# Kernel tuning notes

Hardware: AMD Instinct MI355X
Metric: run time of the kernel (lower is better)

The kernel has to match this reference:

```python
import jax, jax.numpy as jnp
import numpy as np

B, S, D = 4, 4096, 2048
K, H = 64, 32
HD = K // H  # 2
LN_EPS = 1e-5


def setup_inputs() -> dict:
    key = jax.random.key(0)
    ks = jax.random.split(key, 8)
    def xavier(k, shape):
        fan_in, fan_out = shape[1], shape[0]
        lim = float(np.sqrt(6.0 / (fan_in + fan_out)))
        return jax.random.uniform(k, shape, jnp.float32, -lim, lim)
    return {
        "x": jax.random.normal(ks[0], (B, S, D), jnp.float32),
        "norm_w": jnp.ones((D,), jnp.float32),
        "norm_b": jnp.zeros((D,), jnp.float32),
        "qkv_w": xavier(ks[1], (3 * K, D)),
        "qkv_b": jnp.zeros((3 * K,), jnp.float32),
        "fm_w": xavier(ks[2], (HD, HD)),
        "fm_b": jnp.zeros((HD,), jnp.float32),
        "out_w": xavier(ks[3], (D, K)),
        "out_b": jnp.zeros((D,), jnp.float32),
    }


def reference(x, norm_w, norm_b, qkv_w, qkv_b, fm_w, fm_b, out_w, out_b):
    # LayerNorm
    mu = jnp.mean(x, axis=-1, keepdims=True)
    var = jnp.var(x, axis=-1, keepdims=True)
    xn = (x - mu) * jax.lax.rsqrt(var + LN_EPS) * norm_w + norm_b
    # QKV projection: [B,S,3K]
    qkv = xn @ qkv_w.T + qkv_b
    q, k, v = jnp.split(qkv, 3, axis=-1)
    # [B,S,K] -> [B,H,S,hd]
    def heads(t):
        return t.reshape(B, S, H, HD).transpose(0, 2, 1, 3)
    q, k, v = heads(q), heads(k), heads(v)
    # feature map: ReLU(Linear)
    q = jax.nn.relu(q @ fm_w.T + fm_b)
    k = jax.nn.relu(k @ fm_w.T + fm_b)
    # linear attention: kv state [B,H,hd,hd]
    kv = jnp.einsum('bhsd,bhse->bhde', k, v)
    attn = jnp.einsum('bhsd,bhde->bhse', q, kv)
    k_sum = jnp.sum(k, axis=2)                      # [B,H,hd]
    q_k_sum = jnp.einsum('bhsd,bhd->bhs', q, k_sum)[..., None]
    attn = attn / (q_k_sum + 1e-8)
    # merge heads -> [B,S,K]
    attn = attn.transpose(0, 2, 1, 3).reshape(B, S, K)
    out = attn @ out_w.T + out_b
    return x + out
```

## Files before the change

kernel.cpp:

```cpp
#include <hip/hip_runtime.h>
#include <hip/hip_bf16.h>
#include <stdint.h>

typedef unsigned short ushort_t;

#define BB 4
#define SS 4096
#define DD 2048
#define KKC 64
#define HH 32
#define NT (BB*SS)
#define NQKV 192
#define QB 64

#define BUFSZ 40960
#define XOFF  24576

typedef float f32x4 __attribute__((ext_vector_type(4)));
typedef short s16x8 __attribute__((ext_vector_type(8)));

__device__ __forceinline__ ushort_t f2bf(float f) {
    union { float f; uint32_t u; } c; c.f = f;
    uint32_t u = c.u + 0x7fffu + ((c.u >> 16) & 1u);
    return (ushort_t)(u >> 16);
}
__device__ __forceinline__ float bf2f(ushort_t b) {
    union { uint32_t u; float f; } c; c.u = (uint32_t)b << 16; return c.f;
}

__device__ __forceinline__ uint32_t cvtpk(float lo, float hi) {
    uint32_t r;
    asm("v_cvt_pk_bf16_f32 %0, %1, %2" : "=v"(r) : "v"(lo), "v"(hi));
    return r;
}

__device__ __forceinline__ void mfma16(f32x4& d, s16x8 a, s16x8 b) {
    asm volatile("v_mfma_f32_16x16x32_bf16 %0, %1, %2, %0" : "+v"(d) : "v"(a), "v"(b));
}

__device__ __forceinline__ void gload_lds16(const void* gsrc, void* ldst) {
    __builtin_amdgcn_global_load_lds(
        (const __attribute__((address_space(1))) unsigned int*)gsrc,
        (__attribute__((address_space(3))) unsigned int*)ldst,
        16, 0, 0);
}

__global__ __launch_bounds__(256) void k_pre(
    const float* __restrict__ qkv_w, const float* __restrict__ nw,
    const float* __restrict__ out_w,
    ushort_t* __restrict__ W1, ushort_t* __restrict__ W2) {
    int E = blockIdx.x * 256 + threadIdx.x;
    if (E < 49152) {
        int lane = E & 63; int rest = E >> 6;
        int f = rest % 12, g = rest / 12;
        int col = f * 16 + (lane & 15);
        int k0 = g * 32 + 8 * (lane >> 4);
        const float* src = qkv_w + (size_t)col * DD + k0;
        const float* wp = nw + k0;
        union { ushort_t u[8]; uint4 v; } cv;
        #pragma unroll
        for (int e = 0; e < 8; ++e) cv.u[e] = f2bf(src[e] * wp[e]);
        *(uint4*)(W1 + (size_t)E * 8) = cv.v;
    } else {
        int E2 = E - 49152;
        int lane = E2 & 63; int rest = E2 >> 6;
        int kk = rest & 1, F = rest >> 1;
        int n = F * 16 + (lane & 15);
        int k0 = kk * 32 + 8 * (lane >> 4);
        const float* src = out_w + (size_t)n * KKC + k0;
        union { ushort_t u[8]; uint4 v; } cv;
        #pragma unroll
        for (int e = 0; e < 8; ++e) cv.u[e] = f2bf(src[e]);
        *(uint4*)(W2 + (size_t)E2 * 8) = cv.v;
    }
}

__global__ __launch_bounds__(256) void k_colsum(
    const float* __restrict__ qkv_w, const float* __restrict__ nw,
    const float* __restrict__ nb, const float* __restrict__ qkv_b,
    float* __restrict__ S, float* __restrict__ qb2) {
    int col = blockIdx.x * 4 + (threadIdx.x >> 6);
    int lane = threadIdx.x & 63;
    float s = 0.f, qb = 0.f;
    for (int j = 0; j < 32; ++j) {
        int k = j * 64 + lane;
        float w = qkv_w[(size_t)col * DD + k];
        s += bf2f(f2bf(w * nw[k]));
        qb += nb[k] * w;
    }
    #pragma unroll
    for (int off = 32; off >= 1; off >>= 1) {
        s += __shfl_xor(s, off);
        qb += __shfl_xor(qb, off);
    }
    if (lane == 0) { S[col] = s; qb2[col] = qb + qkv_b[col]; }
}

__global__ __launch_bounds__(512) void k_qkv(
    const float* __restrict__ x, const ushort_t* __restrict__ W1,
    const float* __restrict__ S, const float* __restrict__ qb2,
    const float* __restrict__ fm_w, const float* __restrict__ fm_b,
    float* __restrict__ qfeat,
    float* __restrict__ kvpart)
{
    extern __shared__ __align__(16) char dynlds[];
    __shared__ float kvred[32][16][6];
    __shared__ float stats2[2][QB][2];
    __shared__ float stats[QB][2];

    const int tid = threadIdx.x;
    const int wave = tid >> 6, lane = tid & 63;
    const int rg = wave & 3, ch = wave >> 2;
    const int m0 = blockIdx.x * QB;

    const int rloc = rg * 16 + (lane & 15);
    const int q4 = lane >> 4;
    const int swz = rloc & 7;
    const int fbase = ch * 6;

    const int idx0 = wave * 64 + lane;
    const int idx1 = 512 + idx0;
    const int row0 = idx0 >> 4, row1 = idx1 >> 4;
    const size_t xg0 = (size_t)(m0 + row0) * DD + (((idx0 & 15) ^ (row0 & 7)) * 4);
    const size_t xg1 = (size_t)(m0 + row1) * DD + (((idx1 & 15) ^ (row1 & 7)) * 4);
    const int xd0 = idx0 * 16 - lane * 16;
    const int xd1 = idx1 * 16 - lane * 16;

    f32x4 acc[6];
    #pragma unroll
    for (int j = 0; j < 6; ++j) acc[j] = (f32x4){0.f, 0.f, 0.f, 0.f};
    float st1 = 0.f, st2 = 0.f;

#define STAGE(T, OB) do { \
        char* bB_ = dynlds + (OB); \
        char* bX_ = dynlds + (OB) + XOFF; \
        _Pragma("unroll") \
        for (int i_ = 0; i_ < 3; ++i_) { \
            int eb_ = i_ * 512 + wave * 64; \
            gload_lds16((const char*)W1 + ((size_t)(T) * 1536 + eb_ + lane) * 16, \
                        bB_ + eb_ * 16); \
        } \
        gload_lds16(x + xg0 + (size_t)(T) * 64, bX_ + xd0); \
        gload_lds16(x + xg1 + (size_t)(T) * 64, bX_ + xd1); \
    } while (0)

#define STEP_BODY(OC, T) do { \
        const s16x8* bb_ = (const s16x8*)(dynlds + (OC)); \
        const float* xb_ = (const float*)(dynlds + (OC) + XOFF) + rloc * 64; \
        const bool doStats_ = (((T) & 1) == ch); \
        s16x8 afr0_, afr1_; \
        { \
            int sg0_ = 2 * q4, sg1_ = 8 + 2 * q4; \
            float4 a0_ = *(const float4*)(xb_ + ((sg0_    ) ^ swz) * 4); \
            float4 a1_ = *(const float4*)(xb_ + ((sg0_ + 1) ^ swz) * 4); \
            float4 b0_ = *(const float4*)(xb_ + ((sg1_    ) ^ swz) * 4); \
            float4 b1_ = *(const float4*)(xb_ + ((sg1_ + 1) ^ swz) * 4); \
            if (doStats_) { \
                st1 += a0_.x+a0_.y+a0_.z+a0_.w + a1_.x+a1_.y+a1_.z+a1_.w \
                     + b0_.x+b0_.y+b0_.z+b0_.w + b1_.x+b1_.y+b1_.z+b1_.w; \
                st2 += a0_.x*a0_.x+a0_.y*a0_.y+a0_.z*a0_.z+a0_.w*a0_.w \
                     + a1_.x*a1_.x+a1_.y*a1_.y+a1_.z*a1_.z+a1_.w*a1_.w \
                     + b0_.x*b0_.x+b0_.y*b0_.y+b0_.z*b0_.z+b0_.w*b0_.w \
                     + b1_.x*b1_.x+b1_.y*b1_.y+b1_.z*b1_.z+b1_.w*b1_.w; \
            } \
            union { uint32_t w[4]; s16x8 v; } c0_, c1_; \
            c0_.w[0] = cvtpk(a0_.x, a0_.y); c0_.w[1] = cvtpk(a0_.z, a0_.w); \
            c0_.w[2] = cvtpk(a1_.x, a1_.y); c0_.w[3] = cvtpk(a1_.z, a1_.w); \
            c1_.w[0] = cvtpk(b0_.x, b0_.y); c1_.w[1] = cvtpk(b0_.z, b0_.w); \
            c1_.w[2] = cvtpk(b1_.x, b1_.y); c1_.w[3] = cvtpk(b1_.z, b1_.w); \
            afr0_ = c0_.v; afr1_ = c1_.v; \
        } \
        _Pragma("unroll") \
        for (int j_ = 0; j_ < 6; ++j_) { \
            s16x8 w0_ = bb_[(fbase + j_) * 64 + lane]; \
            s16x8 w1_ = bb_[(12 + fbase + j_) * 64 + lane]; \
            mfma16(acc[j_], afr0_, w0_); \
            mfma16(acc[j_], afr1_, w1_); \
        } \
    } while (0)

    STAGE(0, 0);
    STAGE(1, BUFSZ);

    unsigned oc = 0, on = BUFSZ, on2 = 2 * BUFSZ;
    for (int t = 0; t < 31; ++t) {
        asm volatile("s_waitcnt vmcnt(5)" ::: "memory");
        __builtin_amdgcn_s_barrier();
        if (t < 30) STAGE(t + 2, on2);
        STEP_BODY(oc, t);
        unsigned tmp = oc; oc = on; on = on2; on2 = tmp;
    }
    asm volatile("s_waitcnt vmcnt(0)" ::: "memory");
    __builtin_amdgcn_s_barrier();
    STEP_BODY(oc, 31);

    st1 += __shfl_xor(st1, 16); st2 += __shfl_xor(st2, 16);
    st1 += __shfl_xor(st1, 32); st2 += __shfl_xor(st2, 32);
    if (lane < 16) { stats2[ch][rloc][0] = st1; stats2[ch][rloc][1] = st2; }
    __syncthreads();

    float (*cep)[NQKV] = (float (*)[NQKV])dynlds;
    #pragma unroll
    for (int j = 0; j < 6; ++j) {
        int col = (fbase + j) * 16 + (lane & 15);
        int rbase = rg * 16 + (lane >> 4) * 4;
        #pragma unroll
        for (int r = 0; r < 4; ++r)
            cep[rbase + r][col] = acc[j][r];
    }
    if (tid < QB) {
        float s1 = stats2[0][tid][0] + stats2[1][tid][0];
        float s2 = stats2[0][tid][1] + stats2[1][tid][1];
        float mu = s1 * (1.f / DD);
        float var = s2 * (1.f / DD) - mu * mu;
        stats[tid][0] = mu;
        stats[tid][1] = rsqrtf(var + 1e-5f);
    }
    __syncthreads();

    const int h = tid & 31, gg = tid >> 5;
    const float fm00 = fm_w[0], fm01 = fm_w[1], fm10 = fm_w[2], fm11 = fm_w[3];
    const float fb0 = fm_b[0], fb1 = fm_b[1];
    const float Sq0 = S[2*h],      Sq1 = S[2*h+1],      cq0 = qb2[2*h],      cq1 = qb2[2*h+1];
    const float Sk0 = S[64+2*h],   Sk1 = S[64+2*h+1],   ck0 = qb2[64+2*h],   ck1 = qb2[64+2*h+1];
    const float Sv0 = S[128+2*h],  Sv1 = S[128+2*h+1],  cv0 = qb2[128+2*h],  cv1 = qb2[128+2*h+1];
    float kv00=0, kv01=0, kv10=0, kv11=0, ks0=0, ks1=0;
    #pragma unroll
    for (int i = 0; i < 4; ++i) {
        int tt = gg * 4 + i;
        float mu = stats[tt][0], rs = stats[tt][1];
        float f = mu * rs;
        float q0 = rs * cep[tt][2*h]      - f * Sq0 + cq0;
        float q1 = rs * cep[tt][2*h+1]    - f * Sq1 + cq1;
        float k0 = rs * cep[tt][64+2*h]   - f * Sk0 + ck0;
        float k1 = rs * cep[tt][64+2*h+1] - f * Sk1 + ck1;
        float v0 = rs * cep[tt][128+2*h]  - f * Sv0 + cv0;
        float v1 = rs * cep[tt][128+2*h+1]- f * Sv1 + cv1;
        float qp0 = fmaxf(fm00*q0 + fm01*q1 + fb0, 0.f);
        float qp1 = fmaxf(fm10*q0 + fm11*q1 + fb1, 0.f);
        float kp0 = fmaxf(fm00*k0 + fm01*k1 + fb0, 0.f);
        float kp1 = fmaxf(fm10*k0 + fm11*k1 + fb1, 0.f);
        *(float2*)(qfeat + (size_t)(m0 + tt) * KKC + 2*h) = make_float2(qp0, qp1);
        kv00 += kp0*v0; kv01 += kp0*v1; kv10 += kp1*v0; kv11 += kp1*v1;
        ks0 += kp0; ks1 += kp1;
    }
    kvred[h][gg][0]=kv00; kvred[h][gg][1]=kv01; kvred[h][gg][2]=kv10;
    kvred[h][gg][3]=kv11; kvred[h][gg][4]=ks0;  kvred[h][gg][5]=ks1;
    __syncthreads();
    if (tid < 192) {
        int h2 = tid / 6, j = tid % 6;
        float s = 0.f;
        #pragma unroll
        for (int g2 = 0; g2 < 16; ++g2) s += kvred[h2][g2][j];
        kvpart[(size_t)blockIdx.x * 192 + tid] = s;
    }
#undef STAGE
#undef STEP_BODY
}

__global__ void k_red(const float* __restrict__ kvpart, float* __restrict__ kvstate) {
    int idx = blockIdx.x * 256 + threadIdx.x;
    if (idx >= BB * HH * 6) return;
    int b = idx / 192, r = idx % 192;
    float s = 0.f;
    for (int blk = 0; blk < 64; ++blk)
        s += kvpart[(size_t)(b * 64 + blk) * 192 + r];
    kvstate[idx] = s;
}

#define CEP_STRIDE 260
__global__ __launch_bounds__(512, 4) void k_out(
    const float* __restrict__ qfeat, const float* __restrict__ kvstate,
    const ushort_t* __restrict__ W2, const float* __restrict__ out_b,
    const float* __restrict__ x, float* __restrict__ out) {
    __shared__ float skv[192];
    __shared__ __align__(16) float cep[32 * CEP_STRIDE];
    const int tid = threadIdx.x, wave = tid >> 6, lane = tid & 63;
    const int rg = wave & 1, cq = wave >> 1;
    const int mb = blockIdx.x >> 1, nb = blockIdx.x & 1;
    const int m0 = mb * 32;
    const int n0 = nb * 1024;
    const int b = m0 >> 12;
    if (tid < 192) skv[tid] = kvstate[b * 192 + tid];

    const int arow = m0 + rg * 16 + (lane & 15);
    const int ksub = 8 * (lane >> 4);
    float4 qa0 = *(const float4*)(qfeat + (size_t)arow * KKC + ksub);
    float4 qa1 = *(const float4*)(qfeat + (size_t)arow * KKC + ksub + 4);
    float4 qb0 = *(const float4*)(qfeat + (size_t)arow * KKC + 32 + ksub);
    float4 qb1 = *(const float4*)(qfeat + (size_t)arow * KKC + 32 + ksub + 4);
    __syncthreads();

    union { ushort_t u[8]; s16x8 v; } ca, cb;
    {
        float qs[8] = {qa0.x,qa0.y,qa0.z,qa0.w,qa1.x,qa1.y,qa1.z,qa1.w};
        float rs[8] = {qb0.x,qb0.y,qb0.z,qb0.w,qb1.x,qb1.y,qb1.z,qb1.w};
        #pragma unroll
        for (int e = 0; e < 8; e += 2) {
            int h = (ksub + e) >> 1;
            const float* kv = skv + h * 6;
            float q0 = qs[e], q1 = qs[e+1];
            float inv = 1.f / (q0 * kv[4] + q1 * kv[5] + 1e-8f);
            ca.u[e]   = f2bf((q0 * kv[0] + q1 * kv[2]) * inv);
            ca.u[e+1] = f2bf((q0 * kv[1] + q1 * kv[3]) * inv);
            const float* kw = skv + (h + 16) * 6;
            float p0 = rs[e], p1 = rs[e+1];
            float iw = 1.f / (p0 * kw[4] + p1 * kw[5] + 1e-8f);
            cb.u[e]   = f2bf((p0 * kw[0] + p1 * kw[2]) * iw);
            cb.u[e+1] = f2bf((p0 * kw[1] + p1 * kw[3]) * iw);
        }
    }

    f32x4 acc[16];
    #pragma unroll
    for (int j = 0; j < 16; ++j) acc[j] = (f32x4){0.f, 0.f, 0.f, 0.f};
    #pragma unroll
    for (int j = 0; j < 16; ++j) {
        int Fg = (n0 >> 4) + cq + 4 * j;
        s16x8 b0 = *(const s16x8*)(W2 + ((size_t)(Fg * 2 + 0) * 64 + lane) * 8);
        s16x8 b1 = *(const s16x8*)(W2 + ((size_t)(Fg * 2 + 1) * 64 + lane) * 8);
        mfma16(acc[j], ca.v, b0);
        mfma16(acc[j], cb.v, b1);
    }

    const int wrow = rg * 16 + 4 * (lane >> 4);
    #pragma unroll
    for (int n = 0; n < 4; ++n) {
        #pragma unroll
        for (int i = 0; i < 4; ++i) {
            int col = cq * 16 + i * 64 + (lane & 15);
            #pragma unroll
            for (int r = 0; r < 4; ++r)
                cep[(wrow + r) * CEP_STRIDE + col] = acc[4 * n + i][r];
        }
        __syncthreads();
        #pragma unroll
        for (int p = 0; p < 4; ++p) {
            int row = p * 8 + (tid >> 6);
            int c4 = tid & 63;
            float4 c = *(const float4*)(cep + row * CEP_STRIDE + c4 * 4);
            int gcol = n0 + n * 256 + c4 * 4;
            size_t off = (size_t)(m0 + row) * DD + gcol;
            float4 xr = *(const float4*)(x + off);
            float4 ob = *(const float4*)(out_b + gcol);
            float4 o;
            o.x = c.x + ob.x + xr.x; o.y = c.y + ob.y + xr.y;
            o.z = c.z + ob.z + xr.z; o.w = c.w + ob.w + xr.w;
            *(float4*)(out + off) = o;
        }
        __syncthreads();
    }
}

extern "C" void kernel_launch(void* const* d_in, const int* in_sizes, int n_in,
                              void* d_out, int out_size, void* d_ws, size_t ws_size,
                              hipStream_t stream) {
    const float* x     = (const float*)d_in[0];
    const float* nw    = (const float*)d_in[1];
    const float* nb    = (const float*)d_in[2];
    const float* qkv_w = (const float*)d_in[3];
    const float* qkv_b = (const float*)d_in[4];
    const float* fm_w  = (const float*)d_in[5];
    const float* fm_b  = (const float*)d_in[6];
    const float* out_w = (const float*)d_in[7];
    const float* out_b = (const float*)d_in[8];
    float* out = (float*)d_out;

    char* ws = (char*)d_ws;
    ushort_t* W1 = (ushort_t*)ws;     ws += (size_t)NQKV * DD * 2;
    ushort_t* W2 = (ushort_t*)ws;     ws += (size_t)DD * KKC * 2;
    float* qfeat = (float*)ws;        ws += (size_t)NT * KKC * 4;
    float* kvpart = (float*)ws;       ws += (size_t)256 * 192 * 4;
    float* kvstate = (float*)ws;      ws += (size_t)BB * HH * 6 * 4;
    float* Svec = (float*)ws;         ws += (size_t)NQKV * 4;
    float* qb2 = (float*)ws;          ws += (size_t)NQKV * 4;

    hipFuncSetAttribute((const void*)k_qkv,
                        hipFuncAttributeMaxDynamicSharedMemorySize, 3 * BUFSZ);

    k_pre<<<256, 256, 0, stream>>>(qkv_w, nw, out_w, W1, W2);
    k_colsum<<<48, 256, 0, stream>>>(qkv_w, nw, nb, qkv_b, Svec, qb2);
    k_qkv<<<NT / QB, 512, 3 * BUFSZ, stream>>>(x, W1, Svec, qb2, fm_w, fm_b, qfeat, kvpart);
    k_red<<<3, 256, 0, stream>>>(kvpart, kvstate);
    k_out<<<(NT / 32) * 2, 512, 0, stream>>>(qfeat, kvstate, W2, out_b, x, out);
}
```

Baseline: 124.1 us.

## Halve k_qkv row tile to 32 and switch to double-buffered LDS pipeline

Cuts k_qkv's row block from 64 to 32 rows and splits the 192 output columns across 4 wave groups instead of 2. The triple-buffered LDS ring becomes a double buffer with a barrier at the end of each step. Dynamic LDS drops from 120 KB to 64 KB and launch bounds request 4 waves per SIMD, so more blocks can be resident and twice as many blocks are launched. In exchange each block loads the full W1 tile for half as many rows, which doubles W1 traffic per output row, and the pipeline loses one stage of prefetch depth.

Result: no change. 125.7 us (+1.3%).

```diff
diff --git a/kernel.cpp b/kernel.cpp
--- a/kernel.cpp
+++ b/kernel.cpp
@@ -11,10 +11,10 @@
 #define HH 32
 #define NT (BB*SS)
 #define NQKV 192
-#define QB 64
-
-#define BUFSZ 40960
-#define XOFF  24576
+#define QB 32
+
+#define BUF2 32768
+#define XOFF 24576
 
 typedef float f32x4 __attribute__((ext_vector_type(4)));
 typedef short s16x8 __attribute__((ext_vector_type(8)));
@@ -96,7 +96,7 @@
     if (lane == 0) { S[col] = s; qb2[col] = qb + qkv_b[col]; }
 }
 
-__global__ __launch_bounds__(512) void k_qkv(
+__global__ __launch_bounds__(512, 4) void k_qkv(
     const float* __restrict__ x, const ushort_t* __restrict__ W1,
     const float* __restrict__ S, const float* __restrict__ qb2,
     const float* __restrict__ fm_w, const float* __restrict__ fm_b,
@@ -105,30 +105,27 @@
 {
     extern __shared__ __align__(16) char dynlds[];
     __shared__ float kvred[32][16][6];
-    __shared__ float stats2[2][QB][2];
+    __shared__ float stats4[4][QB][2];
     __shared__ float stats[QB][2];
 
     const int tid = threadIdx.x;
     const int wave = tid >> 6, lane = tid & 63;
-    const int rg = wave & 3, ch = wave >> 2;
+    const int rg = wave & 1, ch = wave >> 1;
     const int m0 = blockIdx.x * QB;
 
     const int rloc = rg * 16 + (lane & 15);
     const int q4 = lane >> 4;
     const int swz = rloc & 7;
-    const int fbase = ch * 6;
-
-    const int idx0 = wave * 64 + lane;
-    const int idx1 = 512 + idx0;
-    const int row0 = idx0 >> 4, row1 = idx1 >> 4;
-    const size_t xg0 = (size_t)(m0 + row0) * DD + (((idx0 & 15) ^ (row0 & 7)) * 4);
-    const size_t xg1 = (size_t)(m0 + row1) * DD + (((idx1 & 15) ^ (row1 & 7)) * 4);
-    const int xd0 = idx0 * 16 - lane * 16;
-    const int xd1 = idx1 * 16 - lane * 16;
-
-    f32x4 acc[6];
-    #pragma unroll
-    for (int j = 0; j < 6; ++j) acc[j] = (f32x4){0.f, 0.f, 0.f, 0.f};
+    const int fbase = ch * 3;
+
+    const int row0 = tid >> 4;
+    const int slot0 = (tid & 15) ^ (row0 & 7);
+    const size_t xg0 = (size_t)(m0 + row0) * DD + slot0 * 4;
+    const int xd0 = wave * 1024;
+
+    f32x4 acc[3];
+    #pragma unroll
+    for (int j = 0; j < 3; ++j) acc[j] = (f32x4){0.f, 0.f, 0.f, 0.f};
     float st1 = 0.f, st2 = 0.f;
 
 #define STAGE(T, OB) do { \
@@ -141,13 +138,12 @@
                         bB_ + eb_ * 16); \
         } \
         gload_lds16(x + xg0 + (size_t)(T) * 64, bX_ + xd0); \
-        gload_lds16(x + xg1 + (size_t)(T) * 64, bX_ + xd1); \
     } while (0)
 
 #define STEP_BODY(OC, T) do { \
         const s16x8* bb_ = (const s16x8*)(dynlds + (OC)); \
         const float* xb_ = (const float*)(dynlds + (OC) + XOFF) + rloc * 64; \
-        const bool doStats_ = (((T) & 1) == ch); \
+        const bool doStats_ = (((T) & 3) == ch); \
         s16x8 afr0_, afr1_; \
         { \
             int sg0_ = 2 * q4, sg1_ = 8 + 2 * q4; \
@@ -171,7 +167,7 @@
             afr0_ = c0_.v; afr1_ = c1_.v; \
         } \
         _Pragma("unroll") \
-        for (int j_ = 0; j_ < 6; ++j_) { \
+        for (int j_ = 0; j_ < 3; ++j_) { \
             s16x8 w0_ = bb_[(fbase + j_) * 64 + lane]; \
             s16x8 w1_ = bb_[(12 + fbase + j_) * 64 + lane]; \
             mfma16(acc[j_], afr0_, w0_); \
@@ -180,28 +176,27 @@
     } while (0)
 
     STAGE(0, 0);
-    STAGE(1, BUFSZ);
-
-    unsigned oc = 0, on = BUFSZ, on2 = 2 * BUFSZ;
     for (int t = 0; t < 31; ++t) {
-        asm volatile("s_waitcnt vmcnt(5)" ::: "memory");
+        STAGE(t + 1, ((t + 1) & 1) * BUF2);
+        asm volatile("s_waitcnt vmcnt(4)" ::: "memory");
         __builtin_amdgcn_s_barrier();
-        if (t < 30) STAGE(t + 2, on2);
-        STEP_BODY(oc, t);
-        unsigned tmp = oc; oc = on; on = on2; on2 = tmp;
+        __builtin_amdgcn_sched_barrier(0);
+        STEP_BODY((t & 1) * BUF2, t);
+        __builtin_amdgcn_s_barrier();
     }
     asm volatile("s_waitcnt vmcnt(0)" ::: "memory");
     __builtin_amdgcn_s_barrier();
-    STEP_BODY(oc, 31);
+    __builtin_amdgcn_sched_barrier(0);
+    STEP_BODY((31 & 1) * BUF2, 31);
 
     st1 += __shfl_xor(st1, 16); st2 += __shfl_xor(st2, 16);
     st1 += __shfl_xor(st1, 32); st2 += __shfl_xor(st2, 32);
-    if (lane < 16) { stats2[ch][rloc][0] = st1; stats2[ch][rloc][1] = st2; }
+    if (lane < 16) { stats4[ch][rloc][0] = st1; stats4[ch][rloc][1] = st2; }
     __syncthreads();
 
     float (*cep)[NQKV] = (float (*)[NQKV])dynlds;
     #pragma unroll
-    for (int j = 0; j < 6; ++j) {
+    for (int j = 0; j < 3; ++j) {
         int col = (fbase + j) * 16 + (lane & 15);
         int rbase = rg * 16 + (lane >> 4) * 4;
         #pragma unroll
@@ -209,8 +204,8 @@
             cep[rbase + r][col] = acc[j][r];
     }
     if (tid < QB) {
-        float s1 = stats2[0][tid][0] + stats2[1][tid][0];
-        float s2 = stats2[0][tid][1] + stats2[1][tid][1];
+        float s1 = stats4[0][tid][0] + stats4[1][tid][0] + stats4[2][tid][0] + stats4[3][tid][0];
+        float s2 = stats4[0][tid][1] + stats4[1][tid][1] + stats4[2][tid][1] + stats4[3][tid][1];
         float mu = s1 * (1.f / DD);
         float var = s2 * (1.f / DD) - mu * mu;
         stats[tid][0] = mu;
@@ -226,8 +221,8 @@
     const float Sv0 = S[128+2*h],  Sv1 = S[128+2*h+1],  cv0 = qb2[128+2*h],  cv1 = qb2[128+2*h+1];
     float kv00=0, kv01=0, kv10=0, kv11=0, ks0=0, ks1=0;
     #pragma unroll
-    for (int i = 0; i < 4; ++i) {
-        int tt = gg * 4 + i;
+    for (int i = 0; i < 2; ++i) {
+        int tt = gg * 2 + i;
         float mu = stats[tt][0], rs = stats[tt][1];
         float f = mu * rs;
         float q0 = rs * cep[tt][2*h]      - f * Sq0 + cq0;
@@ -263,8 +258,8 @@
     if (idx >= BB * HH * 6) return;
     int b = idx / 192, r = idx % 192;
     float s = 0.f;
-    for (int blk = 0; blk < 64; ++blk)
-        s += kvpart[(size_t)(b * 64 + blk) * 192 + r];
+    for (int blk = 0; blk < 128; ++blk)
+        s += kvpart[(size_t)(b * 128 + blk) * 192 + r];
     kvstate[idx] = s;
 }
 
@@ -370,17 +365,17 @@
     ushort_t* W1 = (ushort_t*)ws;     ws += (size_t)NQKV * DD * 2;
     ushort_t* W2 = (ushort_t*)ws;     ws += (size_t)DD * KKC * 2;
     float* qfeat = (float*)ws;        ws += (size_t)NT * KKC * 4;
-    float* kvpart = (float*)ws;       ws += (size_t)256 * 192 * 4;
+    float* kvpart = (float*)ws;       ws += (size_t)512 * 192 * 4;
     float* kvstate = (float*)ws;      ws += (size_t)BB * HH * 6 * 4;
     float* Svec = (float*)ws;         ws += (size_t)NQKV * 4;
     float* qb2 = (float*)ws;          ws += (size_t)NQKV * 4;
 
     hipFuncSetAttribute((const void*)k_qkv,
-                        hipFuncAttributeMaxDynamicSharedMemorySize, 3 * BUFSZ);
+                        hipFuncAttributeMaxDynamicSharedMemorySize, 2 * BUF2);
 
     k_pre<<<256, 256, 0, stream>>>(qkv_w, nw, out_w, W1, W2);
     k_colsum<<<48, 256, 0, stream>>>(qkv_w, nw, nb, qkv_b, Svec, qb2);
-    k_qkv<<<NT / QB, 512, 3 * BUFSZ, stream>>>(x, W1, Svec, qb2, fm_w, fm_b, qfeat, kvpart);
+    k_qkv<<<NT / QB, 512, 2 * BUF2, stream>>>(x, W1, Svec, qb2, fm_w, fm_b, qfeat, kvpart);
     k_red<<<3, 256, 0, stream>>>(kvpart, kvstate);
     k_out<<<(NT / 32) * 2, 512, 0, stream>>>(qfeat, kvstate, W2, out_b, x, out);
 }
```
